# Kernel tuning notes

Hardware: AMD Instinct MI355X
Metric: run time of the kernel (lower is better)

## Reference

```python
import jax, jax.numpy as jnp
import numpy as np

NUM_HEADS = 16


def setup_inputs() -> dict:
    key = jax.random.key(0)
    k = jax.random.split(key, 5)
    b, s, h = 2, 2048, 1024
    scale = 1.0 / np.sqrt(h)
    return {
        "x": jax.random.normal(k[0], (b, s, h), dtype=jnp.float32),
        "W_qkv": jax.random.normal(k[1], (h, 3 * h), dtype=jnp.float32) * scale,
        "b_qkv": jax.random.normal(k[2], (3 * h,), dtype=jnp.float32) * 0.02,
        "W_o": jax.random.normal(k[3], (h, h), dtype=jnp.float32) * scale,
        "b_o": jax.random.normal(k[4], (h,), dtype=jnp.float32) * 0.02,
    }


def _mha_causal(Q, K, V, num_heads):
    b, s, hd = Q.shape
    d_head = hd // num_heads
    # b s (n h) -> b n s h
    _Q = Q.reshape(b, s, num_heads, d_head).transpose(0, 2, 1, 3)
    _K = K.reshape(b, s, num_heads, d_head).transpose(0, 2, 1, 3)
    _V = V.reshape(b, s, num_heads, d_head).transpose(0, 2, 1, 3)
    scores = jnp.einsum('bnqh,bnkh->bnqk', _Q, _K)
    causal = jnp.tril(jnp.ones((s, s), dtype=bool))  # True where allowed
    scores = jnp.where(causal, scores, -jnp.inf) / jnp.sqrt(jnp.float32(d_head))
    A = jax.nn.softmax(scores, axis=-1)
    AV = jnp.einsum('bnqk,bnkh->bnqh', A, _V)
    return AV.transpose(0, 2, 1, 3).reshape(b, s, hd)


def reference(x, W_qkv, b_qkv, W_o, b_o):
    qkv = x @ W_qkv + b_qkv  # [b, s, 3h]
    Q, K, V = jnp.split(qkv, 3, axis=-1)
    attn = _mha_causal(Q, K, V, NUM_HEADS)
    return attn @ W_o + b_o
```

## Files before the change

### kernel.cpp

```cpp
#include <hip/hip_runtime.h>
#include <hip/hip_bf16.h>

typedef unsigned short u16;
typedef __attribute__((ext_vector_type(8))) short short8;
typedef __attribute__((ext_vector_type(4))) float f32x4;
typedef __attribute__((ext_vector_type(16))) float f32x16;
typedef __attribute__((ext_vector_type(4))) float float4v;
typedef __attribute__((ext_vector_type(4))) unsigned int uint4v;
typedef __attribute__((ext_vector_type(2))) unsigned int uint2v;

__device__ __forceinline__ u16 f2bf(float f) {
    union { float f; unsigned u; } x;
    x.f = f;
    unsigned r = x.u + 0x7fffu + ((x.u >> 16) & 1u);
    return (u16)(r >> 16);
}

__device__ __forceinline__ unsigned cvtpk(float lo, float hi) {
    unsigned r;
    asm("v_cvt_pk_bf16_f32 %0, %1, %2" : "=v"(r) : "v"(lo), "v"(hi));
    return r;
}

__device__ __forceinline__ void gload16(const u16* g, u16* l) {
    __builtin_amdgcn_global_load_lds(
        (const __attribute__((address_space(1))) unsigned*)g,
        (__attribute__((address_space(3))) unsigned*)l, 16, 0, 0);
}

__global__ __launch_bounds__(256) void cast_f32_bf16(
    const float* __restrict__ src, u16* __restrict__ dst, int n8) {
    int i = blockIdx.x * 256 + threadIdx.x;
    if (i >= n8) return;
    const float4v* s = (const float4v*)(src + (size_t)i * 8);
    float4v a = s[0], b = s[1];
    uint4v o;
    o[0] = (unsigned)f2bf(a[0]) | ((unsigned)f2bf(a[1]) << 16);
    o[1] = (unsigned)f2bf(a[2]) | ((unsigned)f2bf(a[3]) << 16);
    o[2] = (unsigned)f2bf(b[0]) | ((unsigned)f2bf(b[1]) << 16);
    o[3] = (unsigned)f2bf(b[2]) | ((unsigned)f2bf(b[3]) << 16);
    *(uint4v*)(dst + (size_t)i * 8) = o;
}

__global__ __launch_bounds__(256) void transpose_f32_bf16(
    const float* __restrict__ src, u16* __restrict__ dst, int R, int C) {
    __shared__ __align__(16) u16 tile[64][72];
    int tr = blockIdx.x * 64;
    int tc = blockIdx.y * 64;
    int t = threadIdx.x;
    int r = t >> 2;
    int c4 = (t & 3) * 16;
    const float4v* sp = (const float4v*)(src + (size_t)(tr + r) * C + tc + c4);
#pragma unroll
    for (int v = 0; v < 4; v++) {
        float4v x = sp[v];
#pragma unroll
        for (int j = 0; j < 4; j++) tile[r][c4 + v * 4 + j] = f2bf(x[j]);
    }
    __syncthreads();
    u16* dp = dst + (size_t)(tc + r) * R + tr + c4;
#pragma unroll
    for (int i = 0; i < 16; i++) dp[i] = tile[c4 + i][r];
}

__global__ __launch_bounds__(256) void build_kv(
    const u16* __restrict__ qkv, u16* __restrict__ kv) {
    int bh = blockIdx.y;
    int tt = blockIdx.x;
    int b = bh >> 4, h = bh & 15;
    u16* outb = kv + (size_t)bh * 262144 + (size_t)tt * 8192;
    __shared__ __align__(16) u16 tile[64][72];
    int t = threadIdx.x;
    int r = t >> 2;
    int c4 = (t & 3) * 16;
    const u16* srow = qkv + (size_t)(b * 2048 + tt * 64 + r) * 3072 + h * 64;
    *(uint4v*)&outb[r * 64 + c4]     = *(const uint4v*)(srow + 1024 + c4);
    *(uint4v*)&outb[r * 64 + c4 + 8] = *(const uint4v*)(srow + 1024 + c4 + 8);
    *(uint4v*)&tile[r][c4]     = *(const uint4v*)(srow + 2048 + c4);
    *(uint4v*)&tile[r][c4 + 8] = *(const uint4v*)(srow + 2048 + c4 + 8);
    __syncthreads();
    u16* dp = outb + 4096 + r * 64 + c4;
#pragma unroll
    for (int i = 0; i < 16; i++) dp[i] = tile[c4 + i][r];
}

template <bool OUT_BF16>
__global__ __launch_bounds__(256) void gemm_kernel(
    const u16* __restrict__ A, const u16* __restrict__ BT,
    const float* __restrict__ bias, void* __restrict__ Cout,
    int M, int N, int K) {
    __shared__ __align__(16) u16 As[2][128 * 32];
    __shared__ __align__(16) u16 Bs[2][128 * 32];
    int bm = blockIdx.x, bn = blockIdx.y;
    int t = threadIdx.x;
    int lane = t & 63, wave = t >> 6;
    int wr = wave >> 1, wc = wave & 1;
    f32x4 acc[4][4] = {};

    int lrow = lane >> 2;
    int lk = (lane & 3) * 8;
    const u16* gA = A + (size_t)(bm * 128) * K;
    const u16* gB = BT + (size_t)(bn * 128) * K;

    auto stage = [&](int buf, int k0) {
#pragma unroll
        for (int i = 0; i < 2; i++) {
            int ch = wave * 2 + i;
            int row = ch * 16 + lrow;
            gload16(gA + (size_t)row * K + k0 + lk, &As[buf][ch * 512]);
            gload16(gB + (size_t)row * K + k0 + lk, &Bs[buf][ch * 512]);
        }
    };

    stage(0, 0);
    __syncthreads();
    int cur = 0;
    for (int k0 = 0; k0 < K; k0 += 32) {
        if (k0 + 32 < K) stage(cur ^ 1, k0 + 32);
        int row16 = lane & 15, kg = (lane >> 4) * 8;
        short8 af[4], bf[4];
#pragma unroll
        for (int m = 0; m < 4; m++)
            af[m] = *(const short8*)&As[cur][(wr * 64 + m * 16 + row16) * 32 + kg];
#pragma unroll
        for (int n = 0; n < 4; n++)
            bf[n] = *(const short8*)&Bs[cur][(wc * 64 + n * 16 + row16) * 32 + kg];
#pragma unroll
        for (int m = 0; m < 4; m++)
#pragma unroll
            for (int n = 0; n < 4; n++)
                acc[m][n] = __builtin_amdgcn_mfma_f32_16x16x32_bf16(
                    af[m], bf[n], acc[m][n], 0, 0, 0);
        __syncthreads();
        cur ^= 1;
    }

#pragma unroll
    for (int m = 0; m < 4; m++) {
#pragma unroll
        for (int n = 0; n < 4; n++) {
            int col = bn * 128 + wc * 64 + n * 16 + (lane & 15);
            float bv = bias ? bias[col] : 0.f;
#pragma unroll
            for (int r = 0; r < 4; r++) {
                int row = bm * 128 + wr * 64 + m * 16 + (lane >> 4) * 4 + r;
                float v = acc[m][n][r] + bv;
                if constexpr (OUT_BF16)
                    ((u16*)Cout)[(size_t)row * N + col] = f2bf(v);
                else
                    ((float*)Cout)[(size_t)row * N + col] = v;
            }
        }
    }
}

__global__ __launch_bounds__(256, 2) void attn_kernel(
    const u16* __restrict__ qkv, const u16* __restrict__ kv,
    u16* __restrict__ attn) {
    int bid = blockIdx.x;
    int bh = bid & 31;
    int s = bid >> 5;
    int st = (s < 8) ? s : 23 - s;
    int b = bh >> 4, h = bh & 15;
    int t = threadIdx.x;
    int lane = t & 63, w = t >> 6;
    int qb = st * 128 + w * 32;
    int kend = qb + 32;
    int nt = 2 * st + 2;
    int l31 = lane & 31, hi32 = lane >> 5;
    int swz = (lane & 7) << 4;

    __shared__ __align__(16) u16 KVb[24576];

    const u16* kvb = kv + (size_t)bh * 262144;

    auto stage = [&](int buf, int tt) {
        const char* g0 = (const char*)(kvb + (size_t)tt * 8192);
#pragma unroll
        for (int kv2 = 0; kv2 < 2; kv2++)
#pragma unroll
            for (int i = 0; i < 2; i++) {
                int o = i * 4096 + t * 16;
                int row = o >> 7;
                int cb = (o & 127) ^ ((row & 7) << 4);
                gload16((const u16*)(g0 + kv2 * 8192 + row * 128 + cb),
                        &KVb[buf * 8192 + kv2 * 4096 + i * 2048 + (t & 192) * 8]);
            }
    };

    short8 qf[4];
    {
        const u16* q0 = qkv + (size_t)(b * 2048 + qb + l31) * 3072 + h * 64 + hi32 * 8;
#pragma unroll
        for (int dd = 0; dd < 4; dd++) qf[dd] = *(const short8*)(q0 + dd * 16);
    }
    stage(0, 0);
    stage(1, 1);

    float l_lane = 0.f;
    f32x16 oT[2] = {};

    const float C1 = 0.1803368880f;
    const float C2 = -17.3123404907f;

    asm volatile("s_waitcnt vmcnt(4)" ::: "memory");
    __builtin_amdgcn_sched_barrier(0);
    __builtin_amdgcn_s_barrier();
    __builtin_amdgcn_sched_barrier(0);

    for (int tt = 0; tt < nt; tt++) {
        bool pre = (tt + 2 < nt);
        if (pre) stage((tt + 2) % 3, tt + 2);
        int k0 = tt * 64;
        if (k0 < kend) {
            const u16* Ks = &KVb[(tt % 3) * 8192];
            const u16* Vs = Ks + 4096;

            f32x16 sc[2];
            __builtin_amdgcn_s_setprio(1);
#pragma unroll
            for (int kb = 0; kb < 2; kb++) {
                f32x16 z = {};
#pragma unroll
                for (int dd = 0; dd < 4; dd++) {
                    int off = (kb * 32 + l31) * 64 + (((dd * 32 + hi32 * 16) ^ swz) >> 1);
                    short8 kf = *(const short8*)&Ks[off];
                    z = __builtin_amdgcn_mfma_f32_32x32x16_bf16(kf, qf[dd], z, 0, 0, 0);
                }
                sc[kb] = z;
            }
            __builtin_amdgcn_s_setprio(0);

            float p[2][16];
            int q_g = qb + l31;
            if (k0 + 64 > qb) {
#pragma unroll
                for (int kb = 0; kb < 2; kb++)
#pragma unroll
                    for (int r = 0; r < 16; r++) {
                        int kg = k0 + kb * 32 + (r & 3) + 8 * (r >> 2) + 4 * hi32;
                        float v = (kg <= q_g) ? sc[kb][r] : -1e30f;
                        float pe = __builtin_amdgcn_exp2f(fmaf(v, C1, C2));
                        p[kb][r] = pe;
                        l_lane += pe;
                    }
            } else {
#pragma unroll
                for (int kb = 0; kb < 2; kb++)
#pragma unroll
                    for (int r = 0; r < 16; r++) {
                        float pe = __builtin_amdgcn_exp2f(fmaf(sc[kb][r], C1, C2));
                        p[kb][r] = pe;
                        l_lane += pe;
                    }
            }

            short8 pb[4];
#pragma unroll
            for (int kb = 0; kb < 2; kb++)
#pragma unroll
                for (int cset = 0; cset < 2; cset++) {
                    const float* pp = &p[kb][cset * 8];
                    unsigned A0 = cvtpk(pp[0], pp[1]);
                    unsigned A1 = cvtpk(pp[2], pp[3]);
                    unsigned A2 = cvtpk(pp[4], pp[5]);
                    unsigned A3 = cvtpk(pp[6], pp[7]);
                    unsigned za = hi32 ? A0 : A2;
                    unsigned zb = hi32 ? A1 : A3;
                    unsigned sa = (unsigned)__shfl_xor((int)za, 32, 64);
                    unsigned sb = (unsigned)__shfl_xor((int)zb, 32, 64);
                    uint4v wv;
                    wv[0] = hi32 ? sa : A0;
                    wv[1] = hi32 ? sb : A1;
                    wv[2] = hi32 ? A2 : sa;
                    wv[3] = hi32 ? A3 : sb;
                    pb[kb * 2 + cset] = __builtin_bit_cast(short8, wv);
                }

            __builtin_amdgcn_s_setprio(1);
#pragma unroll
            for (int mb = 0; mb < 2; mb++)
#pragma unroll
                for (int kk = 0; kk < 4; kk++) {
                    int off = (mb * 32 + l31) * 64 + (((kk * 32 + hi32 * 16) ^ swz) >> 1);
                    short8 vf = *(const short8*)&Vs[off];
                    oT[mb] = __builtin_amdgcn_mfma_f32_32x32x16_bf16(vf, pb[kk], oT[mb], 0, 0, 0);
                }
            __builtin_amdgcn_s_setprio(0);
        }
        if (pre) { asm volatile("s_waitcnt vmcnt(4)" ::: "memory"); }
        else     { asm volatile("s_waitcnt vmcnt(0)" ::: "memory"); }
        __builtin_amdgcn_sched_barrier(0);
        __builtin_amdgcn_s_barrier();
        __builtin_amdgcn_sched_barrier(0);
    }

    float lf = l_lane + __shfl_xor(l_lane, 32, 64);
    float linv = __builtin_amdgcn_rcpf(lf);

    u16* ob = &KVb[w * 2304];
#pragma unroll
    for (int mb = 0; mb < 2; mb++)
#pragma unroll
        for (int rr = 0; rr < 4; rr++) {
            unsigned w0 = cvtpk(oT[mb][4 * rr] * linv, oT[mb][4 * rr + 1] * linv);
            unsigned w1 = cvtpk(oT[mb][4 * rr + 2] * linv, oT[mb][4 * rr + 3] * linv);
            int d0 = mb * 32 + rr * 8 + 4 * hi32;
            *(uint2v*)&ob[l31 * 72 + d0] = (uint2v){w0, w1};
        }
    {
        const u16* rp = &ob[l31 * 72 + hi32 * 32];
        u16* gp = attn + (size_t)(b * 2048 + qb + l31) * 1024 + h * 64 + hi32 * 32;
#pragma unroll
        for (int i = 0; i < 4; i++)
            *(uint4v*)(gp + i * 8) = *(const uint4v*)(rp + i * 8);
    }
}

extern "C" void kernel_launch(void* const* d_in, const int* in_sizes, int n_in,
                              void* d_out, int out_size, void* d_ws, size_t ws_size,
                              hipStream_t stream) {
    const float* x    = (const float*)d_in[0];
    const float* Wqkv = (const float*)d_in[1];
    const float* bqkv = (const float*)d_in[2];
    const float* Wo   = (const float*)d_in[3];
    const float* bo   = (const float*)d_in[4];
    float* out = (float*)d_out;

    char* ws = (char*)d_ws;
    u16* x_bf  = (u16*)(ws);
    u16* attnb = (u16*)(ws);
    u16* wqkvT = (u16*)(ws + (8ull << 20));
    u16* woT   = (u16*)(ws + (14ull << 20));
    u16* qkv   = (u16*)(ws + (16ull << 20));
    u16* kvp   = (u16*)(ws + (40ull << 20));

    cast_f32_bf16<<<2048, 256, 0, stream>>>(x, x_bf, 4096 * 1024 / 8);
    transpose_f32_bf16<<<dim3(16, 48), 256, 0, stream>>>(Wqkv, wqkvT, 1024, 3072);
    transpose_f32_bf16<<<dim3(16, 16), 256, 0, stream>>>(Wo, woT, 1024, 1024);
    gemm_kernel<true><<<dim3(32, 24), 256, 0, stream>>>(
        x_bf, wqkvT, bqkv, (void*)qkv, 4096, 3072, 1024);
    build_kv<<<dim3(32, 32), 256, 0, stream>>>(qkv, kvp);
    attn_kernel<<<512, 256, 0, stream>>>(qkv, kvp, attnb);
    gemm_kernel<false><<<dim3(32, 8), 256, 0, stream>>>(
        attnb, woT, bo, (void*)out, 4096, 1024, 1024);
}
```

Baseline: 123.0 us.

## Add triple-buffered swizzled GEMM, split-K attention for long rows, smaller output tiles

The GEMM moves from double to triple buffering with XOR-swizzled LDS staging, explicit vmcnt waits, raw barriers and MFMA priority. It also gains a template tile width so the output projection uses 64-wide tiles, doubling its block count. The attention kernel splits the longer query tiles (sp>=8) into two key-range halves that write fp32 partial outputs and row sums, and a new merge kernel combines them. This is meant to balance causal work across more blocks, at the cost of extra fp32 partial traffic and one more launch.

```diff
diff --git a/kernel.cpp b/kernel.cpp
--- a/kernel.cpp
+++ b/kernel.cpp
@@ -27,6 +27,8 @@
         (const __attribute__((address_space(1))) unsigned*)g,
         (__attribute__((address_space(3))) unsigned*)l, 16, 0, 0);
 }
+
+#define WAITV(n) asm volatile("s_waitcnt vmcnt(" #n ")" ::: "memory")
 
 __global__ __launch_bounds__(256) void cast_f32_bf16(
     const float* __restrict__ src, u16* __restrict__ dst, int n8) {
@@ -84,62 +86,84 @@
     for (int i = 0; i < 16; i++) dp[i] = tile[c4 + i][r];
 }
 
-template <bool OUT_BF16>
+template <int BN, bool OUT_BF16>
 __global__ __launch_bounds__(256) void gemm_kernel(
     const u16* __restrict__ A, const u16* __restrict__ BT,
     const float* __restrict__ bias, void* __restrict__ Cout,
     int M, int N, int K) {
-    __shared__ __align__(16) u16 As[2][128 * 32];
-    __shared__ __align__(16) u16 Bs[2][128 * 32];
+    constexpr int NF = BN / 32;
+    __shared__ __align__(16) u16 As[3][128 * 32];
+    __shared__ __align__(16) u16 Bs[3][BN * 32];
     int bm = blockIdx.x, bn = blockIdx.y;
     int t = threadIdx.x;
     int lane = t & 63, wave = t >> 6;
     int wr = wave >> 1, wc = wave & 1;
-    f32x4 acc[4][4] = {};
-
-    int lrow = lane >> 2;
-    int lk = (lane & 3) * 8;
+    f32x4 acc[4][NF] = {};
+
     const u16* gA = A + (size_t)(bm * 128) * K;
-    const u16* gB = BT + (size_t)(bn * 128) * K;
+    const u16* gB = BT + (size_t)(bn * BN) * K;
 
     auto stage = [&](int buf, int k0) {
 #pragma unroll
         for (int i = 0; i < 2; i++) {
-            int ch = wave * 2 + i;
-            int row = ch * 16 + lrow;
-            gload16(gA + (size_t)row * K + k0 + lk, &As[buf][ch * 512]);
-            gload16(gB + (size_t)row * K + k0 + lk, &Bs[buf][ch * 512]);
+            int o = i * 4096 + t * 16;
+            int row = o >> 6;
+            int cb = (o & 63) ^ (((row >> 1) & 3) << 4);
+            gload16(gA + (size_t)row * K + k0 + (cb >> 1),
+                    &As[buf][i * 2048 + (t & 192) * 8]);
+        }
+#pragma unroll
+        for (int i = 0; i < BN / 64; i++) {
+            int o = i * 4096 + t * 16;
+            int row = o >> 6;
+            int cb = (o & 63) ^ (((row >> 1) & 3) << 4);
+            gload16(gB + (size_t)row * K + k0 + (cb >> 1),
+                    &Bs[buf][i * 2048 + (t & 192) * 8]);
         }
     };
 
     stage(0, 0);
-    __syncthreads();
-    int cur = 0;
-    for (int k0 = 0; k0 < K; k0 += 32) {
-        if (k0 + 32 < K) stage(cur ^ 1, k0 + 32);
-        int row16 = lane & 15, kg = (lane >> 4) * 8;
-        short8 af[4], bf[4];
+    stage(1, 32);
+    if constexpr (BN == 128) WAITV(4); else WAITV(3);
+    __builtin_amdgcn_sched_barrier(0);
+    __builtin_amdgcn_s_barrier();
+    __builtin_amdgcn_sched_barrier(0);
+
+    int nk = K >> 5;
+    for (int tt = 0; tt < nk; tt++) {
+        bool pre = (tt + 2 < nk);
+        if (pre) stage((tt + 2) % 3, (tt + 2) << 5);
+        int row16 = lane & 15;
+        int colb = ((lane >> 4) * 16) ^ (((row16 >> 1) & 3) << 4);
+        const u16* Ab = As[tt % 3];
+        const u16* Bb = Bs[tt % 3];
+        short8 af[4], bf[NF];
 #pragma unroll
         for (int m = 0; m < 4; m++)
-            af[m] = *(const short8*)&As[cur][(wr * 64 + m * 16 + row16) * 32 + kg];
-#pragma unroll
-        for (int n = 0; n < 4; n++)
-            bf[n] = *(const short8*)&Bs[cur][(wc * 64 + n * 16 + row16) * 32 + kg];
+            af[m] = *(const short8*)&Ab[(wr * 64 + m * 16 + row16) * 32 + (colb >> 1)];
+#pragma unroll
+        for (int n = 0; n < NF; n++)
+            bf[n] = *(const short8*)&Bb[(wc * (BN / 2) + n * 16 + row16) * 32 + (colb >> 1)];
+        __builtin_amdgcn_s_setprio(1);
 #pragma unroll
         for (int m = 0; m < 4; m++)
 #pragma unroll
-            for (int n = 0; n < 4; n++)
+            for (int n = 0; n < NF; n++)
                 acc[m][n] = __builtin_amdgcn_mfma_f32_16x16x32_bf16(
                     af[m], bf[n], acc[m][n], 0, 0, 0);
-        __syncthreads();
-        cur ^= 1;
+        __builtin_amdgcn_s_setprio(0);
+        if (pre) { if constexpr (BN == 128) WAITV(4); else WAITV(3); }
+        else     { WAITV(0); }
+        __builtin_amdgcn_sched_barrier(0);
+        __builtin_amdgcn_s_barrier();
+        __builtin_amdgcn_sched_barrier(0);
     }
 
 #pragma unroll
     for (int m = 0; m < 4; m++) {
 #pragma unroll
-        for (int n = 0; n < 4; n++) {
-            int col = bn * 128 + wc * 64 + n * 16 + (lane & 15);
+        for (int n = 0; n < NF; n++) {
+            int col = bn * BN + wc * (BN / 2) + n * 16 + (lane & 15);
             float bv = bias ? bias[col] : 0.f;
 #pragma unroll
             for (int r = 0; r < 4; r++) {
@@ -156,17 +180,32 @@
 
 __global__ __launch_bounds__(256, 2) void attn_kernel(
     const u16* __restrict__ qkv, const u16* __restrict__ kv,
-    u16* __restrict__ attn) {
+    u16* __restrict__ attn, float* __restrict__ part_o,
+    float* __restrict__ part_l) {
     int bid = blockIdx.x;
     int bh = bid & 31;
-    int s = bid >> 5;
-    int st = (s < 8) ? s : 23 - s;
+    int j = 23 - (bid >> 5);
+    int sp, tbeg, tend, kc = 0;
+    bool partial;
+    if (j >= 8) {
+        int idx = j - 8;
+        sp = 8 + (idx >> 1);
+        kc = idx & 1;
+        int half = sp + 1;
+        partial = true;
+        tbeg = kc ? half : 0;
+        tend = kc ? 2 * sp + 2 : half;
+    } else {
+        sp = j;
+        partial = false;
+        tbeg = 0;
+        tend = 2 * sp + 2;
+    }
     int b = bh >> 4, h = bh & 15;
     int t = threadIdx.x;
     int lane = t & 63, w = t >> 6;
-    int qb = st * 128 + w * 32;
+    int qb = sp * 128 + w * 32;
     int kend = qb + 32;
-    int nt = 2 * st + 2;
     int l31 = lane & 31, hi32 = lane >> 5;
     int swz = (lane & 7) << 4;
 
@@ -194,8 +233,8 @@
 #pragma unroll
         for (int dd = 0; dd < 4; dd++) qf[dd] = *(const short8*)(q0 + dd * 16);
     }
-    stage(0, 0);
-    stage(1, 1);
+    stage(tbeg % 3, tbeg);
+    stage((tbeg + 1) % 3, tbeg + 1);
 
     float l_lane = 0.f;
     f32x16 oT[2] = {};
@@ -203,19 +242,18 @@
     const float C1 = 0.1803368880f;
     const float C2 = -17.3123404907f;
 
-    asm volatile("s_waitcnt vmcnt(4)" ::: "memory");
+    WAITV(4);
     __builtin_amdgcn_sched_barrier(0);
     __builtin_amdgcn_s_barrier();
     __builtin_amdgcn_sched_barrier(0);
 
-    for (int tt = 0; tt < nt; tt++) {
-        bool pre = (tt + 2 < nt);
+    for (int tt = tbeg; tt < tend; tt++) {
+        bool pre = (tt + 2 < tend);
         if (pre) stage((tt + 2) % 3, tt + 2);
         int k0 = tt * 64;
         if (k0 < kend) {
             const u16* Ks = &KVb[(tt % 3) * 8192];
             const u16* Vs = Ks + 4096;
-
             f32x16 sc[2];
             __builtin_amdgcn_s_setprio(1);
 #pragma unroll
@@ -288,16 +326,30 @@
                 }
             __builtin_amdgcn_s_setprio(0);
         }
-        if (pre) { asm volatile("s_waitcnt vmcnt(4)" ::: "memory"); }
-        else     { asm volatile("s_waitcnt vmcnt(0)" ::: "memory"); }
+        if (pre) { WAITV(4); } else { WAITV(0); }
         __builtin_amdgcn_sched_barrier(0);
         __builtin_amdgcn_s_barrier();
         __builtin_amdgcn_sched_barrier(0);
     }
 
+    if (partial) {
+        int blk = (bh * 8 + (sp - 8)) * 2 + kc;
+        float* po = part_o + (size_t)blk * 8192;
+        int lr = w * 32 + l31;
+        float lf = l_lane + __shfl_xor(l_lane, 32, 64);
+        if (hi32 == 0) part_l[blk * 128 + lr] = lf;
+#pragma unroll
+        for (int mb = 0; mb < 2; mb++)
+#pragma unroll
+            for (int r = 0; r < 16; r++) {
+                int d = mb * 32 + (r & 3) + 8 * (r >> 2) + 4 * hi32;
+                po[lr * 64 + d] = oT[mb][r];
+            }
+        return;
+    }
+
     float lf = l_lane + __shfl_xor(l_lane, 32, 64);
     float linv = __builtin_amdgcn_rcpf(lf);
-
     u16* ob = &KVb[w * 2304];
 #pragma unroll
     for (int mb = 0; mb < 2; mb++)
@@ -317,6 +369,37 @@
     }
 }
 
+__global__ __launch_bounds__(256) void attn_merge(
+    const float* __restrict__ part_o, const float* __restrict__ part_l,
+    u16* __restrict__ attn) {
+    int bid = blockIdx.x;
+    int bh = bid & 31;
+    int sp8 = bid >> 5;
+    int sp = sp8 + 8;
+    int b = bh >> 4, h = bh & 15;
+    int t = threadIdx.x;
+    int blk0 = (bh * 8 + sp8) * 2;
+    const float* o0 = part_o + (size_t)blk0 * 8192;
+    const float* o1 = o0 + 8192;
+    const float* l0 = part_l + blk0 * 128;
+    const float* l1 = l0 + 128;
+#pragma unroll
+    for (int i = 0; i < 4; i++) {
+        int r = (t >> 3) + i * 32;
+        int d0 = (t & 7) * 8;
+        float linv = __builtin_amdgcn_rcpf(l0[r] + l1[r]);
+        const float* a = o0 + r * 64 + d0;
+        const float* c = o1 + r * 64 + d0;
+        uint4v w;
+#pragma unroll
+        for (int k = 0; k < 4; k++)
+            w[k] = cvtpk((a[2 * k] + c[2 * k]) * linv,
+                         (a[2 * k + 1] + c[2 * k + 1]) * linv);
+        u16* gp = attn + (size_t)(b * 2048 + sp * 128 + r) * 1024 + h * 64 + d0;
+        *(uint4v*)gp = w;
+    }
+}
+
 extern "C" void kernel_launch(void* const* d_in, const int* in_sizes, int n_in,
                               void* d_out, int out_size, void* d_ws, size_t ws_size,
                               hipStream_t stream) {
@@ -328,20 +411,23 @@
     float* out = (float*)d_out;
 
     char* ws = (char*)d_ws;
-    u16* x_bf  = (u16*)(ws);
-    u16* attnb = (u16*)(ws);
-    u16* wqkvT = (u16*)(ws + (8ull << 20));
-    u16* woT   = (u16*)(ws + (14ull << 20));
-    u16* qkv   = (u16*)(ws + (16ull << 20));
-    u16* kvp   = (u16*)(ws + (40ull << 20));
+    u16* x_bf   = (u16*)(ws);
+    u16* attnb  = (u16*)(ws);
+    u16* wqkvT  = (u16*)(ws + (8ull << 20));
+    u16* woT    = (u16*)(ws + (14ull << 20));
+    u16* qkv    = (u16*)(ws + (16ull << 20));
+    u16* kvp    = (u16*)(ws + (40ull << 20));
+    float* part_o = (float*)(ws + (58ull << 20));
+    float* part_l = (float*)(ws + (74ull << 20));
 
     cast_f32_bf16<<<2048, 256, 0, stream>>>(x, x_bf, 4096 * 1024 / 8);
     transpose_f32_bf16<<<dim3(16, 48), 256, 0, stream>>>(Wqkv, wqkvT, 1024, 3072);
     transpose_f32_bf16<<<dim3(16, 16), 256, 0, stream>>>(Wo, woT, 1024, 1024);
-    gemm_kernel<true><<<dim3(32, 24), 256, 0, stream>>>(
+    gemm_kernel<128, true><<<dim3(32, 24), 256, 0, stream>>>(
         x_bf, wqkvT, bqkv, (void*)qkv, 4096, 3072, 1024);
     build_kv<<<dim3(32, 32), 256, 0, stream>>>(qkv, kvp);
-    attn_kernel<<<512, 256, 0, stream>>>(qkv, kvp, attnb);
-    gemm_kernel<false><<<dim3(32, 8), 256, 0, stream>>>(
+    attn_kernel<<<768, 256, 0, stream>>>(qkv, kvp, attnb, part_o, part_l);
+    attn_merge<<<256, 256, 0, stream>>>(part_o, part_l, attnb);
+    gemm_kernel<64, false><<<dim3(32, 16), 256, 0, stream>>>(
         attnb, woT, bo, (void*)out, 4096, 1024, 1024);
 }
```

Measured after the change: 121.5 us. Within noise of the previous version (-1.2%).
